# Kernel tuning notes

Measured on AMD Instinct MI355X. Metric: run time of the kernel, lower is better.

The kernel has to match this reference:

```python
import jax, jax.numpy as jnp
import numpy as np

CORNER_MASK = jnp.array(
    [[0, 0, 0], [0, 0, 1], [0, 1, 0], [0, 1, 1],
     [1, 0, 0], [1, 0, 1], [1, 1, 0], [1, 1, 1]], dtype=jnp.float32)


def setup_inputs() -> dict:
    key = jax.random.key(0)
    k1, k2, k3, k4 = jax.random.split(key, 4)
    DEPTH = 6
    G = 2 ** DEPTH            # 64 voxels per axis at depth 6
    C = 32                    # feature channels
    H = G * G * G             # 262144 octree nodes at depth 6
    N = 1_000_000             # query points (depth-7 node centers)

    data = jax.random.normal(k1, (1, C, H, 1), dtype=jnp.float32)
    # points scaled into [0, 2^depth]; last column is the batch id (single octree -> 0)
    xyz = jax.random.uniform(k2, (N, 3), dtype=jnp.float32) * G
    ids = jnp.zeros((N, 1), dtype=jnp.float32)
    pts = jnp.concatenate([xyz, ids], axis=1)

    # dense voxel -> node-index lookup emulating ocnn.octree_search_key;
    idx_grid = jax.random.randint(k3, (G, G, G), 0, H, dtype=jnp.int32)
    empty = jax.random.uniform(k4, (G, G, G)) < 0.1
    lut = jnp.where(empty, jnp.int32(-1), idx_grid)

    return {"data": data, "pts": pts, "lut": lut, "depth": DEPTH}


def reference(data, pts, lut, depth):
    # data: (1, C, H, 1); pts: (N, 4); lut: (G, G, G) int32; depth: python int
    G = 2 ** depth
    xyzf = pts[:, :3] - 0.5                      # (N, 3)
    xyzi = jnp.floor(xyzf)
    frac = xyzf - xyzi                           # (N, 3) fractional offsets

    corners = xyzi[:, None, :] + CORNER_MASK[None, :, :]   # (N, 8, 3)
    ci = corners.astype(jnp.int32)
    in_bounds = jnp.all((ci >= 0) & (ci < G), axis=-1)     # (N, 8)
    ci_safe = jnp.clip(ci, 0, G - 1)
    idx = lut[ci_safe[..., 0], ci_safe[..., 1], ci_safe[..., 2]]  # (N, 8)
    valid = in_bounds & (idx > -1)

    # trilinear weights: |prod((1 - mask) - frac)|, matching the torch code
    w = jnp.abs(jnp.prod((1.0 - CORNER_MASK)[None, :, :] - frac[:, None, :], axis=-1))
    w = jnp.where(valid, w, 0.0)                 # (N, 8)
    idx_safe = jnp.where(valid, idx, 0)

    feat = data[0, :, :, 0].T                    # (H, C)
    gathered = feat[idx_safe]                    # (N, 8, C)
    out = jnp.einsum('nk,nkc->nc', w, gathered)  # weighted accumulate
    norm = jnp.sum(w, axis=1, keepdims=True)     # (N, 1)
    out = out / (norm + 1e-10)
    return out.T[None, :, :, None]               # (1, C, N, 1)
```

## Files before the change

### kernel.cpp

```cpp
#include <hip/hip_runtime.h>
#include <hip/hip_fp16.h>


#define NCH 32

typedef float nvec4 __attribute__((ext_vector_type(4)));

__global__ __launch_bounds__(256) void octri_transpose_h(
    const float* __restrict__ data, __half* __restrict__ featH, int H) {
  __shared__ float tile[32][33];
  const int h0 = blockIdx.x * 32;
  const int tx = threadIdx.x;
  const int ty = threadIdx.y;
#pragma unroll
  for (int i = 0; i < 4; ++i) {
    int c = ty + 8 * i;
    tile[c][tx] =
        __builtin_nontemporal_load(&data[(size_t)c * H + h0 + tx]);
  }
  __syncthreads();
#pragma unroll
  for (int i = 0; i < 4; ++i) {
    int hl = ty + 8 * i;
    featH[(size_t)(h0 + hl) * NCH + tx] = __float2half(tile[tx][hl]);
  }
}

__global__ __launch_bounds__(256) void octri_voxelize(
    const __half* __restrict__ featH, const int* __restrict__ lut,
    __half* __restrict__ featV, unsigned long long* __restrict__ vmask) {
  const int t = threadIdx.x;
  const int zi = t >> 2;
  const int j = t & 3;
  const int v = blockIdx.x * 64 + zi;
  const int id = lut[v];

  nvec4 row = {0.f, 0.f, 0.f, 0.f};
  if (id >= 0)
    row = *(const nvec4*)(featH + ((size_t)id << 5) + (j << 3));
  *(nvec4*)(featV + ((size_t)v << 5) + (j << 3)) = row;

  const unsigned long long b = __ballot(id >= 0);
  unsigned int comp = 0;
#pragma unroll
  for (int k = 0; k < 16; ++k)
    comp |= ((unsigned)(b >> (4 * k)) & 1u) << k;
  __shared__ unsigned short sm16[4];
  if ((t & 63) == 0) sm16[t >> 6] = (unsigned short)comp;
  __syncthreads();
  if (t == 0) {
    unsigned long long m = (unsigned long long)sm16[0] |
                           ((unsigned long long)sm16[1] << 16) |
                           ((unsigned long long)sm16[2] << 32) |
                           ((unsigned long long)sm16[3] << 48);
    vmask[blockIdx.x] = m;
  }
}

__global__ __launch_bounds__(256) void octri_gather3(
    const __half* __restrict__ featV,
    const unsigned long long* __restrict__ vmask,
    const float* __restrict__ pts, const int* __restrict__ depth_p,
    float* __restrict__ out, int N) {
  __shared__ int meta[256][17];

  const int pblk = blockIdx.x * 256;
  const int G = 1 << depth_p[0];
  const int G1 = G - 1;

  {
    const int p = threadIdx.x;
    const int n = min(pblk + p, N - 1);
    const nvec4 pt =
        __builtin_nontemporal_load((const nvec4*)(pts + (size_t)n * 4));
    const float fx = pt.x - 0.5f, fy = pt.y - 0.5f, fz = pt.z - 0.5f;
    const float flx = floorf(fx), fly = floorf(fy), flz = floorf(fz);
    const int ix = (int)flx, iy = (int)fly, iz = (int)flz;
    const float rx = fx - flx, ry = fy - fly, rz = fz - flz;
    const float wx[2] = {1.f - rx, rx};
    const float wy[2] = {1.f - ry, ry};
    const float wz[2] = {1.f - rz, rz};
    const bool vx[2] = {(unsigned)ix < (unsigned)G,
                        (unsigned)(ix + 1) < (unsigned)G};
    const bool vy[2] = {(unsigned)iy < (unsigned)G,
                        (unsigned)(iy + 1) < (unsigned)G};
    const bool vz[2] = {(unsigned)iz < (unsigned)G,
                        (unsigned)(iz + 1) < (unsigned)G};
    const int cxc[2] = {min(max(ix, 0), G1), min(max(ix + 1, 0), G1)};
    const int cyc[2] = {min(max(iy, 0), G1), min(max(iy + 1, 0), G1)};
    const int czc[2] = {min(max(iz, 0), G1), min(max(iz + 1, 0), G1)};

    unsigned long long mrow[2][2];
#pragma unroll
    for (int bx = 0; bx < 2; ++bx)
#pragma unroll
      for (int by = 0; by < 2; ++by)
        mrow[bx][by] = vmask[cxc[bx] * G + cyc[by]];

    int vv[8];
    float w[8], wsum = 0.f;
#pragma unroll
    for (int k = 0; k < 8; ++k) {
      const int bx = (k >> 2) & 1, by = (k >> 1) & 1, bz = k & 1;
      const bool valid = vx[bx] && vy[by] && vz[bz] &&
                         (((mrow[bx][by] >> czc[bz]) & 1ull) != 0);
      vv[k] = (cxc[bx] * G + cyc[by]) * G + czc[bz];
      float wk = wx[bx] * wy[by] * wz[bz];
      wk = valid ? wk : 0.f;
      w[k] = wk;
      wsum += wk;
    }
    const float s = (pblk + p < N) ? (1.f / (wsum + 1e-10f)) : 0.f;
#pragma unroll
    for (int k = 0; k < 8; ++k) {
      meta[p][k] = vv[k];
      meta[p][8 + k] = __float_as_int(w[k] * s);
    }
  }
  __syncthreads();

  const int lane = threadIdx.x & 63;
  const int wid = threadIdx.x >> 6;
  const int j = lane & 3;
#pragma unroll
  for (int g = 0; g < 4; ++g) {
    const int p = (wid << 6) + (g << 4) + (lane >> 2);
    const int n = pblk + p;

    nvec4 r[8];
    float ws[8];
#pragma unroll
    for (int k = 0; k < 8; ++k) {
      const int v = meta[p][k];
      ws[k] = __int_as_float(meta[p][8 + k]);
      r[k] = *(const nvec4*)(featV + ((size_t)v << 5) + (j << 3));
    }
    float acc[8] = {};
#pragma unroll
    for (int k = 0; k < 8; ++k) {
      const __half2* h2 = (const __half2*)&r[k];
#pragma unroll
      for (int q = 0; q < 4; ++q) {
        const float2 f = __half22float2(h2[q]);
        acc[2 * q + 0] += ws[k] * f.x;
        acc[2 * q + 1] += ws[k] * f.y;
      }
    }
    if (n < N) {
#pragma unroll
      for (int q = 0; q < 8; ++q) {
        __builtin_nontemporal_store(acc[q],
                                    &out[(size_t)(8 * j + q) * N + n]);
      }
    }
  }
}

__global__ __launch_bounds__(256) void octri_gather2(
    const __half* __restrict__ featH,
    const float* __restrict__ pts, const int* __restrict__ lut,
    const int* __restrict__ depth_p, float* __restrict__ out, int N) {
  __shared__ int meta[256][17];
  const int pblk = blockIdx.x * 256;
  const int G = 1 << depth_p[0];

  {
    const int p = threadIdx.x;
    const int n = min(pblk + p, N - 1);
    const nvec4 pt =
        __builtin_nontemporal_load((const nvec4*)(pts + (size_t)n * 4));
    const float fx = pt.x - 0.5f, fy = pt.y - 0.5f, fz = pt.z - 0.5f;
    const float flx = floorf(fx), fly = floorf(fy), flz = floorf(fz);
    const int ix = (int)flx, iy = (int)fly, iz = (int)flz;
    const float rx = fx - flx, ry = fy - fly, rz = fz - flz;
    const float wx[2] = {1.f - rx, rx};
    const float wy[2] = {1.f - ry, ry};
    const float wz[2] = {1.f - rz, rz};
    const bool vx[2] = {(unsigned)ix < (unsigned)G,
                        (unsigned)(ix + 1) < (unsigned)G};
    const bool vy[2] = {(unsigned)iy < (unsigned)G,
                        (unsigned)(iy + 1) < (unsigned)G};
    const bool vz[2] = {(unsigned)iz < (unsigned)G,
                        (unsigned)(iz + 1) < (unsigned)G};

    int idx[8];
    float w[8], wsum = 0.f;
#pragma unroll
    for (int k = 0; k < 8; ++k) {
      const int bx = (k >> 2) & 1, by = (k >> 1) & 1, bz = k & 1;
      const bool inb = vx[bx] & vy[by] & vz[bz];
      int id = -1;
      if (inb)
        id = lut[((size_t)(ix + bx) * G + (iy + by)) * G + (iz + bz)];
      const bool valid = inb && (id > -1);
      float wk = wx[bx] * wy[by] * wz[bz];
      wk = valid ? wk : 0.f;
      idx[k] = valid ? id : 0;
      w[k] = wk;
      wsum += wk;
    }
    const float s = (pblk + p < N) ? (1.f / (wsum + 1e-10f)) : 0.f;
#pragma unroll
    for (int k = 0; k < 8; ++k) {
      meta[p][k] = idx[k];
      meta[p][8 + k] = __float_as_int(w[k] * s);
    }
  }
  __syncthreads();

  const int lane = threadIdx.x & 63;
  const int wid = threadIdx.x >> 6;
  const int j = lane & 3;
#pragma unroll
  for (int g = 0; g < 4; ++g) {
    const int p = (wid << 6) + (g << 4) + (lane >> 2);
    const int n = pblk + p;

    float acc[8] = {};
#pragma unroll
    for (int k = 0; k < 8; ++k) {
      const int id = meta[p][k];
      const float ws = __int_as_float(meta[p][8 + k]);
      const nvec4 hv = *(const nvec4*)(featH + (size_t)id * NCH + j * 8);
      const __half2* h2 = (const __half2*)&hv;
#pragma unroll
      for (int q = 0; q < 4; ++q) {
        const float2 f = __half22float2(h2[q]);
        acc[2 * q + 0] += ws * f.x;
        acc[2 * q + 1] += ws * f.y;
      }
    }
    if (n < N) {
#pragma unroll
      for (int q = 0; q < 8; ++q) {
        __builtin_nontemporal_store(acc[q],
                                    &out[(size_t)(8 * j + q) * N + n]);
      }
    }
  }
}

__global__ __launch_bounds__(256) void octri_gather_direct(
    const float* __restrict__ data, const float* __restrict__ pts,
    const int* __restrict__ lut, const int* __restrict__ depth_p,
    float* __restrict__ out, int N, int H) {
  const int n = blockIdx.x * blockDim.x + threadIdx.x;
  if (n >= N) return;
  const int G = 1 << depth_p[0];

  const float4 p = ((const float4*)pts)[n];
  const float fx = p.x - 0.5f, fy = p.y - 0.5f, fz = p.z - 0.5f;
  const float flx = floorf(fx), fly = floorf(fy), flz = floorf(fz);
  const int ix = (int)flx, iy = (int)fly, iz = (int)flz;
  const float rx = fx - flx, ry = fy - fly, rz = fz - flz;
  const float wx[2] = {1.f - rx, rx};
  const float wy[2] = {1.f - ry, ry};
  const float wz[2] = {1.f - rz, rz};

  int idx[8];
  float w[8], wsum = 0.f;
#pragma unroll
  for (int k = 0; k < 8; ++k) {
    const int bx = (k >> 2) & 1, by = (k >> 1) & 1, bz = k & 1;
    const int cx = ix + bx, cy = iy + by, cz = iz + bz;
    const bool inb = (cx >= 0) & (cx < G) & (cy >= 0) & (cy < G) &
                     (cz >= 0) & (cz < G);
    int id = -1;
    if (inb) id = lut[((size_t)cx * G + cy) * G + cz];
    const bool valid = inb && (id > -1);
    float wk = wx[bx] * wy[by] * wz[bz];
    wk = valid ? wk : 0.f;
    idx[k] = valid ? id : 0;
    w[k] = wk;
    wsum += wk;
  }

  const float s = 1.f / (wsum + 1e-10f);
#pragma unroll 4
  for (int c = 0; c < NCH; ++c) {
    const float* plane = data + (size_t)c * H;
    float a = 0.f;
#pragma unroll
    for (int k = 0; k < 8; ++k) a += w[k] * plane[idx[k]];
    out[(size_t)c * N + n] = a * s;
  }
}

extern "C" void kernel_launch(void* const* d_in, const int* in_sizes, int n_in,
                              void* d_out, int out_size, void* d_ws,
                              size_t ws_size, hipStream_t stream) {
  const float* data = (const float*)d_in[0];
  const float* pts = (const float*)d_in[1];
  const int* lut = (const int*)d_in[2];
  const int* depth_p = (const int*)d_in[3];
  float* out = (float*)d_out;

  const int H = in_sizes[0] / NCH;
  const int N = in_sizes[1] / 4;
  const int SV = in_sizes[2];

  int G = 1;
  while ((size_t)(G + 1) * (G + 1) * (G + 1) <= (size_t)SV) ++G;

  const size_t featH_bytes = (size_t)H * NCH * sizeof(__half);
  const size_t featV_bytes = (size_t)SV * NCH * sizeof(__half);
  const size_t needV = featV_bytes + (size_t)G * G * sizeof(unsigned long long);

  if (G == 64 && (size_t)G * G * G == (size_t)SV && (H % 32) == 0 &&
      ws_size >= needV &&
      featH_bytes <= (size_t)out_size * sizeof(float)) {
    __half* featH = (__half*)d_out;
    __half* featV = (__half*)d_ws;
    unsigned long long* vmask =
        (unsigned long long*)((char*)d_ws + featV_bytes);
    dim3 tb(32, 8);
    octri_transpose_h<<<H / 32, tb, 0, stream>>>(data, featH, H);
    octri_voxelize<<<SV / 64, 256, 0, stream>>>(featH, lut, featV, vmask);
    const int blocks = (N + 255) / 256;
    octri_gather3<<<blocks, 256, 0, stream>>>(featV, vmask, pts, depth_p,
                                              out, N);
  } else if (ws_size >= featH_bytes && (H % 32) == 0) {
    __half* featH = (__half*)d_ws;
    dim3 tb(32, 8);
    octri_transpose_h<<<H / 32, tb, 0, stream>>>(data, featH, H);
    const int blocks = (N + 255) / 256;
    octri_gather2<<<blocks, 256, 0, stream>>>(featH, pts, lut, depth_p, out,
                                              N);
  } else {
    octri_gather_direct<<<(N + 255) / 256, 256, 0, stream>>>(
        data, pts, lut, depth_p, out, N, H);
  }
}
```

Before: 261.6 us.

## Bin query points by x-slab before gathering to improve voxel cache locality

Adds a counting-sort pipeline (count, scan, scatter) that groups points into 8 x-slabs. The gather kernel then processes each slab so the featV rows it touches stay in a smaller working set, writing fp16 results to a temporary buffer. An unpermute kernel scatters the results back to the original order through LDS and writes the fp32 channel-major output. This trades several extra launches and extra passes over the points and temporary results for better cache hit rates on the random voxel gathers. The fp16 intermediate also adds rounding error.

```diff
diff --git a/kernel.cpp b/kernel.cpp
--- a/kernel.cpp
+++ b/kernel.cpp
@@ -3,6 +3,8 @@
 
 
 #define NCH 32
+#define BIN_W 512
+#define NGRP 8
 
 typedef float nvec4 __attribute__((ext_vector_type(4)));
 
@@ -15,8 +17,7 @@
 #pragma unroll
   for (int i = 0; i < 4; ++i) {
     int c = ty + 8 * i;
-    tile[c][tx] =
-        __builtin_nontemporal_load(&data[(size_t)c * H + h0 + tx]);
+    tile[c][tx] = __builtin_nontemporal_load(&data[(size_t)c * H + h0 + tx]);
   }
   __syncthreads();
 #pragma unroll
@@ -36,8 +37,7 @@
   const int id = lut[v];
 
   nvec4 row = {0.f, 0.f, 0.f, 0.f};
-  if (id >= 0)
-    row = *(const nvec4*)(featH + ((size_t)id << 5) + (j << 3));
+  if (id >= 0) row = *(const nvec4*)(featH + ((size_t)id << 5) + (j << 3));
   *(nvec4*)(featV + ((size_t)v << 5) + (j << 3)) = row;
 
   const unsigned long long b = __ballot(id >= 0);
@@ -57,17 +57,273 @@
   }
 }
 
+__global__ __launch_bounds__(256) void octri_bin_count(
+    const float* __restrict__ pts, int N, int NB, int* __restrict__ counts) {
+  __shared__ int cnt[NGRP];
+  if (threadIdx.x < NGRP) cnt[threadIdx.x] = 0;
+  __syncthreads();
+  const int b = blockIdx.x;
+#pragma unroll
+  for (int i = 0; i < 2; ++i) {
+    const int n = b * BIN_W + i * 256 + threadIdx.x;
+    if (n < N) {
+      const nvec4 pt =
+          __builtin_nontemporal_load((const nvec4*)(pts + (size_t)n * 4));
+      const int ix = (int)floorf(pt.x - 0.5f);
+      const int g = min(max(ix, 0), 63) >> 3;
+      atomicAdd(&cnt[g], 1);
+    }
+  }
+  __syncthreads();
+  if (threadIdx.x < NGRP) counts[threadIdx.x * NB + b] = cnt[threadIdx.x];
+}
+
+__global__ __launch_bounds__(256) void octri_bin_scan(
+    const int* __restrict__ counts, int* __restrict__ bases, int M) {
+  extern __shared__ int buf[];
+  const int t = threadIdx.x;
+  const int seg = (M + 255) / 256;
+  for (int i = t; i < M; i += 256) buf[i] = counts[i];
+  __syncthreads();
+  int* stot = buf + M;
+  {
+    int s = 0;
+    const int lo = t * seg, hi = min(lo + seg, M);
+    for (int i = lo; i < hi; ++i) { int c = buf[i]; buf[i] = s; s += c; }
+    stot[t] = s;
+  }
+  __syncthreads();
+  if (t == 0) {
+    int s = 0;
+    for (int i = 0; i < 256; ++i) { int c = stot[i]; stot[i] = s; s += c; }
+  }
+  __syncthreads();
+  {
+    const int add = stot[t];
+    const int lo = t * seg, hi = min(lo + seg, M);
+    for (int i = lo; i < hi; ++i) bases[i] = buf[i] + add;
+  }
+}
+
+__global__ __launch_bounds__(256) void octri_bin_scatter(
+    const float* __restrict__ pts, int N, int NB, const int* __restrict__ bases,
+    float* __restrict__ binned, int* __restrict__ inv) {
+  __shared__ int run[NGRP];
+  __shared__ int wcnt[4][NGRP];
+  __shared__ int woff[4][NGRP];
+  const int b = blockIdx.x;
+  const int t = threadIdx.x;
+  const int lane = t & 63, wid = t >> 6;
+  if (t < NGRP) run[t] = bases[t * NB + b];
+  __syncthreads();
+#pragma unroll
+  for (int i = 0; i < 2; ++i) {
+    if (t < 32) wcnt[t >> 3][t & 7] = 0;
+    __syncthreads();
+    const int n = b * BIN_W + i * 256 + t;
+    const bool act = (n < N);
+    nvec4 pt = {0.f, 0.f, 0.f, 0.f};
+    int g = 0;
+    if (act) {
+      pt = __builtin_nontemporal_load((const nvec4*)(pts + (size_t)n * 4));
+      g = min(max((int)floorf(pt.x - 0.5f), 0), 63) >> 3;
+    }
+    unsigned long long m = 0;
+#pragma unroll
+    for (int gg = 0; gg < NGRP; ++gg) {
+      const unsigned long long bm = __ballot(act && (g == gg));
+      if (gg == g) m = bm;
+    }
+    const unsigned long long ltm = (1ull << lane) - 1ull;
+    const int rank = __popcll(m & ltm);
+    if (act && rank == 0) wcnt[wid][g] = __popcll(m);
+    __syncthreads();
+    if (t < NGRP) {
+      int r = run[t];
+#pragma unroll
+      for (int w = 0; w < 4; ++w) { woff[w][t] = r; r += wcnt[w][t]; }
+      run[t] = r;
+    }
+    __syncthreads();
+    if (act) {
+      const int slot = woff[wid][g] + rank;
+      __builtin_nontemporal_store(pt, (nvec4*)(binned + (size_t)slot * 4));
+      inv[n] = slot;
+    }
+    __syncthreads();
+  }
+}
+
+__global__ __launch_bounds__(256) void octri_gather4(
+    const __half* __restrict__ featV, const unsigned long long* __restrict__ vmask,
+    const float* __restrict__ binned, const int* __restrict__ bases, int NB,
+    int N, int CPB, __half* __restrict__ temp) {
+  __shared__ int meta[256][17];
+  const int g = blockIdx.x & 7;
+  const int Gb0 = bases[g * NB];
+  const int Gb1 = (g < 7) ? bases[(g + 1) * NB] : N;
+  const int G = 64, G1 = 63;
+
+  for (int chunk = blockIdx.x >> 3;; chunk += CPB) {
+    const int s0 = Gb0 + (chunk << 8);
+    if (s0 >= Gb1) break;
+    const int cnt = min(256, Gb1 - s0);
+
+    {
+      const int p = threadIdx.x;
+      const int s = s0 + min(p, cnt - 1);
+      const nvec4 pt =
+          __builtin_nontemporal_load((const nvec4*)(binned + (size_t)s * 4));
+      const float fx = pt.x - 0.5f, fy = pt.y - 0.5f, fz = pt.z - 0.5f;
+      const float flx = floorf(fx), fly = floorf(fy), flz = floorf(fz);
+      const int ix = (int)flx, iy = (int)fly, iz = (int)flz;
+      const float rx = fx - flx, ry = fy - fly, rz = fz - flz;
+      const float wx[2] = {1.f - rx, rx};
+      const float wy[2] = {1.f - ry, ry};
+      const float wz[2] = {1.f - rz, rz};
+      const bool vx[2] = {(unsigned)ix < (unsigned)G,
+                          (unsigned)(ix + 1) < (unsigned)G};
+      const bool vy[2] = {(unsigned)iy < (unsigned)G,
+                          (unsigned)(iy + 1) < (unsigned)G};
+      const bool vz[2] = {(unsigned)iz < (unsigned)G,
+                          (unsigned)(iz + 1) < (unsigned)G};
+      const int cxc[2] = {min(max(ix, 0), G1), min(max(ix + 1, 0), G1)};
+      const int cyc[2] = {min(max(iy, 0), G1), min(max(iy + 1, 0), G1)};
+      const int czc[2] = {min(max(iz, 0), G1), min(max(iz + 1, 0), G1)};
+
+      unsigned long long mrow[2][2];
+#pragma unroll
+      for (int bx = 0; bx < 2; ++bx)
+#pragma unroll
+        for (int by = 0; by < 2; ++by)
+          mrow[bx][by] = vmask[cxc[bx] * G + cyc[by]];
+
+      int vv[8];
+      float w[8], wsum = 0.f;
+#pragma unroll
+      for (int k = 0; k < 8; ++k) {
+        const int bx = (k >> 2) & 1, by = (k >> 1) & 1, bz = k & 1;
+        const bool valid = vx[bx] && vy[by] && vz[bz] &&
+                           (((mrow[bx][by] >> czc[bz]) & 1ull) != 0);
+        vv[k] = (cxc[bx] * G + cyc[by]) * G + czc[bz];
+        float wk = wx[bx] * wy[by] * wz[bz];
+        wk = valid ? wk : 0.f;
+        w[k] = wk;
+        wsum += wk;
+      }
+      const float sc = (p < cnt) ? (1.f / (wsum + 1e-10f)) : 0.f;
+#pragma unroll
+      for (int k = 0; k < 8; ++k) {
+        meta[p][k] = vv[k];
+        meta[p][8 + k] = __float_as_int(w[k] * sc);
+      }
+    }
+    __syncthreads();
+
+    const int lane = threadIdx.x & 63;
+    const int wid = threadIdx.x >> 6;
+    const int j = lane & 3;
+#pragma unroll
+    for (int gq = 0; gq < 4; ++gq) {
+      const int p = (wid << 6) + (gq << 4) + (lane >> 2);
+
+      nvec4 r[8];
+      float ws[8];
+#pragma unroll
+      for (int k = 0; k < 8; ++k) {
+        const int v = meta[p][k];
+        ws[k] = __int_as_float(meta[p][8 + k]);
+        r[k] = *(const nvec4*)(featV + ((size_t)v << 5) + (j << 3));
+      }
+      float acc[8] = {};
+#pragma unroll
+      for (int k = 0; k < 8; ++k) {
+        const __half2* h2 = (const __half2*)&r[k];
+#pragma unroll
+        for (int q = 0; q < 4; ++q) {
+          const float2 f = __half22float2(h2[q]);
+          acc[2 * q + 0] += ws[k] * f.x;
+          acc[2 * q + 1] += ws[k] * f.y;
+        }
+      }
+      if (p < cnt) {
+        union { __half2 h2[4]; nvec4 v; } u;
+#pragma unroll
+        for (int q = 0; q < 4; ++q)
+          u.h2[q] = __floats2half2_rn(acc[2 * q], acc[2 * q + 1]);
+        __builtin_nontemporal_store(
+            u.v, (nvec4*)(temp + ((size_t)(s0 + p) << 5) + (j << 3)));
+      }
+    }
+    __syncthreads();
+  }
+}
+
+__global__ __launch_bounds__(256) void octri_unpermute(
+    const __half* __restrict__ temp, const int* __restrict__ inv,
+    const int* __restrict__ bases, int NB, int N, float* __restrict__ out) {
+  __shared__ __half rows[BIN_W * NCH];
+  __shared__ int cur[NGRP], off[NGRP + 1], Gb[NGRP + 1];
+  const int b = blockIdx.x;
+  const int t = threadIdx.x;
+  if (t < NGRP) {
+    const int c0 = bases[t * NB + b];
+    const int c1 = (b + 1 < NB) ? bases[t * NB + b + 1]
+                                : ((t < 7) ? bases[(t + 1) * NB] : N);
+    cur[t] = c0;
+    off[t] = c1 - c0;
+    Gb[t] = bases[t * NB];
+  }
+  if (t == 0) Gb[NGRP] = N;
+  __syncthreads();
+  if (t == 0) {
+    int s = 0;
+#pragma unroll
+    for (int gg = 0; gg < NGRP; ++gg) { int l = off[gg]; off[gg] = s; s += l; }
+    off[NGRP] = s;
+  }
+  __syncthreads();
+  for (int gg = 0; gg < NGRP; ++gg) {
+    const int len4 = (off[gg + 1] - off[gg]) << 2;
+    const nvec4* src = (const nvec4*)(temp + ((size_t)cur[gg] << 5));
+    nvec4* dst = (nvec4*)(rows + ((size_t)off[gg] << 5));
+    for (int k = t; k < len4; k += 256)
+      dst[k] = __builtin_nontemporal_load(src + k);
+  }
+  __syncthreads();
+#pragma unroll
+  for (int i = 0; i < 2; ++i) {
+    const int n = b * BIN_W + i * 256 + t;
+    if (n < N) {
+      const int slot = inv[n];
+      int gg = 0;
+      while (slot >= Gb[gg + 1]) ++gg;
+      const int r = slot - cur[gg] + off[gg];
+      const __half* hp = rows + ((size_t)r << 5);
+#pragma unroll
+      for (int k = 0; k < 4; ++k) {
+        const nvec4 hv = *(const nvec4*)(hp + (k << 3));
+        const __half2* h2 = (const __half2*)&hv;
+#pragma unroll
+        for (int q = 0; q < 4; ++q) {
+          const float2 f = __half22float2(h2[q]);
+          __builtin_nontemporal_store(f.x, &out[(size_t)(k * 8 + 2 * q) * N + n]);
+          __builtin_nontemporal_store(f.y,
+                                      &out[(size_t)(k * 8 + 2 * q + 1) * N + n]);
+        }
+      }
+    }
+  }
+}
+
 __global__ __launch_bounds__(256) void octri_gather3(
-    const __half* __restrict__ featV,
-    const unsigned long long* __restrict__ vmask,
+    const __half* __restrict__ featV, const unsigned long long* __restrict__ vmask,
     const float* __restrict__ pts, const int* __restrict__ depth_p,
     float* __restrict__ out, int N) {
   __shared__ int meta[256][17];
-
   const int pblk = blockIdx.x * 256;
   const int G = 1 << depth_p[0];
   const int G1 = G - 1;
-
   {
     const int p = threadIdx.x;
     const int n = min(pblk + p, N - 1);
@@ -89,14 +345,12 @@
     const int cxc[2] = {min(max(ix, 0), G1), min(max(ix + 1, 0), G1)};
     const int cyc[2] = {min(max(iy, 0), G1), min(max(iy + 1, 0), G1)};
     const int czc[2] = {min(max(iz, 0), G1), min(max(iz + 1, 0), G1)};
-
     unsigned long long mrow[2][2];
 #pragma unroll
     for (int bx = 0; bx < 2; ++bx)
 #pragma unroll
       for (int by = 0; by < 2; ++by)
         mrow[bx][by] = vmask[cxc[bx] * G + cyc[by]];
-
     int vv[8];
     float w[8], wsum = 0.f;
 #pragma unroll
@@ -118,7 +372,6 @@
     }
   }
   __syncthreads();
-
   const int lane = threadIdx.x & 63;
   const int wid = threadIdx.x >> 6;
   const int j = lane & 3;
@@ -126,7 +379,6 @@
   for (int g = 0; g < 4; ++g) {
     const int p = (wid << 6) + (g << 4) + (lane >> 2);
     const int n = pblk + p;
-
     nvec4 r[8];
     float ws[8];
 #pragma unroll
@@ -148,94 +400,8 @@
     }
     if (n < N) {
 #pragma unroll
-      for (int q = 0; q < 8; ++q) {
-        __builtin_nontemporal_store(acc[q],
-                                    &out[(size_t)(8 * j + q) * N + n]);
-      }
-    }
-  }
-}
-
-__global__ __launch_bounds__(256) void octri_gather2(
-    const __half* __restrict__ featH,
-    const float* __restrict__ pts, const int* __restrict__ lut,
-    const int* __restrict__ depth_p, float* __restrict__ out, int N) {
-  __shared__ int meta[256][17];
-  const int pblk = blockIdx.x * 256;
-  const int G = 1 << depth_p[0];
-
-  {
-    const int p = threadIdx.x;
-    const int n = min(pblk + p, N - 1);
-    const nvec4 pt =
-        __builtin_nontemporal_load((const nvec4*)(pts + (size_t)n * 4));
-    const float fx = pt.x - 0.5f, fy = pt.y - 0.5f, fz = pt.z - 0.5f;
-    const float flx = floorf(fx), fly = floorf(fy), flz = floorf(fz);
-    const int ix = (int)flx, iy = (int)fly, iz = (int)flz;
-    const float rx = fx - flx, ry = fy - fly, rz = fz - flz;
-    const float wx[2] = {1.f - rx, rx};
-    const float wy[2] = {1.f - ry, ry};
-    const float wz[2] = {1.f - rz, rz};
-    const bool vx[2] = {(unsigned)ix < (unsigned)G,
-                        (unsigned)(ix + 1) < (unsigned)G};
-    const bool vy[2] = {(unsigned)iy < (unsigned)G,
-                        (unsigned)(iy + 1) < (unsigned)G};
-    const bool vz[2] = {(unsigned)iz < (unsigned)G,
-                        (unsigned)(iz + 1) < (unsigned)G};
-
-    int idx[8];
-    float w[8], wsum = 0.f;
-#pragma unroll
-    for (int k = 0; k < 8; ++k) {
-      const int bx = (k >> 2) & 1, by = (k >> 1) & 1, bz = k & 1;
-      const bool inb = vx[bx] & vy[by] & vz[bz];
-      int id = -1;
-      if (inb)
-        id = lut[((size_t)(ix + bx) * G + (iy + by)) * G + (iz + bz)];
-      const bool valid = inb && (id > -1);
-      float wk = wx[bx] * wy[by] * wz[bz];
-      wk = valid ? wk : 0.f;
-      idx[k] = valid ? id : 0;
-      w[k] = wk;
-      wsum += wk;
-    }
-    const float s = (pblk + p < N) ? (1.f / (wsum + 1e-10f)) : 0.f;
-#pragma unroll
-    for (int k = 0; k < 8; ++k) {
-      meta[p][k] = idx[k];
-      meta[p][8 + k] = __float_as_int(w[k] * s);
-    }
-  }
-  __syncthreads();
-
-  const int lane = threadIdx.x & 63;
-  const int wid = threadIdx.x >> 6;
-  const int j = lane & 3;
-#pragma unroll
-  for (int g = 0; g < 4; ++g) {
-    const int p = (wid << 6) + (g << 4) + (lane >> 2);
-    const int n = pblk + p;
-
-    float acc[8] = {};
-#pragma unroll
-    for (int k = 0; k < 8; ++k) {
-      const int id = meta[p][k];
-      const float ws = __int_as_float(meta[p][8 + k]);
-      const nvec4 hv = *(const nvec4*)(featH + (size_t)id * NCH + j * 8);
-      const __half2* h2 = (const __half2*)&hv;
-#pragma unroll
-      for (int q = 0; q < 4; ++q) {
-        const float2 f = __half22float2(h2[q]);
-        acc[2 * q + 0] += ws * f.x;
-        acc[2 * q + 1] += ws * f.y;
-      }
-    }
-    if (n < N) {
-#pragma unroll
-      for (int q = 0; q < 8; ++q) {
-        __builtin_nontemporal_store(acc[q],
-                                    &out[(size_t)(8 * j + q) * N + n]);
-      }
+      for (int q = 0; q < 8; ++q)
+        __builtin_nontemporal_store(acc[q], &out[(size_t)(8 * j + q) * N + n]);
     }
   }
 }
@@ -247,7 +413,6 @@
   const int n = blockIdx.x * blockDim.x + threadIdx.x;
   if (n >= N) return;
   const int G = 1 << depth_p[0];
-
   const float4 p = ((const float4*)pts)[n];
   const float fx = p.x - 0.5f, fy = p.y - 0.5f, fz = p.z - 0.5f;
   const float flx = floorf(fx), fly = floorf(fy), flz = floorf(fz);
@@ -256,15 +421,14 @@
   const float wx[2] = {1.f - rx, rx};
   const float wy[2] = {1.f - ry, ry};
   const float wz[2] = {1.f - rz, rz};
-
   int idx[8];
   float w[8], wsum = 0.f;
 #pragma unroll
   for (int k = 0; k < 8; ++k) {
     const int bx = (k >> 2) & 1, by = (k >> 1) & 1, bz = k & 1;
     const int cx = ix + bx, cy = iy + by, cz = iz + bz;
-    const bool inb = (cx >= 0) & (cx < G) & (cy >= 0) & (cy < G) &
-                     (cz >= 0) & (cz < G);
+    const bool inb = (cx >= 0) & (cx < G) & (cy >= 0) & (cy < G) & (cz >= 0) &
+                     (cz < G);
     int id = -1;
     if (inb) id = lut[((size_t)cx * G + cy) * G + cz];
     const bool valid = inb && (id > -1);
@@ -274,7 +438,6 @@
     w[k] = wk;
     wsum += wk;
   }
-
   const float s = 1.f / (wsum + 1e-10f);
 #pragma unroll 4
   for (int c = 0; c < NCH; ++c) {
@@ -302,13 +465,58 @@
   int G = 1;
   while ((size_t)(G + 1) * (G + 1) * (G + 1) <= (size_t)SV) ++G;
 
+  const int NB = (N + BIN_W - 1) / BIN_W;
+  const int M = NGRP * NB;
+
   const size_t featH_bytes = (size_t)H * NCH * sizeof(__half);
   const size_t featV_bytes = (size_t)SV * NCH * sizeof(__half);
-  const size_t needV = featV_bytes + (size_t)G * G * sizeof(unsigned long long);
+
+  size_t offw = 0;
+  auto alloc = [&](size_t bytes) {
+    offw = (offw + 255) & ~(size_t)255;
+    size_t o = offw;
+    offw += bytes;
+    return o;
+  };
+  const size_t o_featV = alloc(featV_bytes);
+  const size_t o_vmask = alloc((size_t)G * G * sizeof(unsigned long long));
+  const size_t o_binned = alloc((size_t)NB * BIN_W * 16);
+  const size_t o_temp = alloc((size_t)NB * BIN_W * NCH * sizeof(__half));
+  const size_t o_inv = alloc((size_t)NB * BIN_W * sizeof(int));
+  const size_t o_counts = alloc((size_t)M * sizeof(int));
+  const size_t o_bases = alloc((size_t)M * sizeof(int));
+  const size_t need_full = offw;
+
+  const size_t scan_lds = (size_t)(M + 256) * sizeof(int);
+  const size_t needV =
+      featV_bytes + (size_t)G * G * sizeof(unsigned long long);
 
   if (G == 64 && (size_t)G * G * G == (size_t)SV && (H % 32) == 0 &&
-      ws_size >= needV &&
+      ws_size >= need_full && scan_lds <= 150 * 1024 &&
       featH_bytes <= (size_t)out_size * sizeof(float)) {
+    char* ws = (char*)d_ws;
+    __half* featH = (__half*)d_out;
+    __half* featV = (__half*)(ws + o_featV);
+    unsigned long long* vmask = (unsigned long long*)(ws + o_vmask);
+    float* binned = (float*)(ws + o_binned);
+    __half* temp = (__half*)(ws + o_temp);
+    int* inv = (int*)(ws + o_inv);
+    int* counts = (int*)(ws + o_counts);
+    int* bases = (int*)(ws + o_bases);
+
+    dim3 tb(32, 8);
+    octri_transpose_h<<<H / 32, tb, 0, stream>>>(data, featH, H);
+    octri_voxelize<<<SV / 64, 256, 0, stream>>>(featH, lut, featV, vmask);
+    octri_bin_count<<<NB, 256, 0, stream>>>(pts, N, NB, counts);
+    octri_bin_scan<<<1, 256, scan_lds, stream>>>(counts, bases, M);
+    octri_bin_scatter<<<NB, 256, 0, stream>>>(pts, N, NB, bases, binned, inv);
+    const int CPB = (N / NGRP + 1024) / 1024 * 5 + 8;
+    octri_gather4<<<NGRP * CPB, 256, 0, stream>>>(featV, vmask, binned, bases,
+                                                  NB, N, CPB, temp);
+    octri_unpermute<<<NB, 256, 0, stream>>>(temp, inv, bases, NB, N, out);
+  } else if (G == 64 && (size_t)G * G * G == (size_t)SV && (H % 32) == 0 &&
+             ws_size >= needV &&
+             featH_bytes <= (size_t)out_size * sizeof(float)) {
     __half* featH = (__half*)d_out;
     __half* featV = (__half*)d_ws;
     unsigned long long* vmask =
@@ -316,16 +524,8 @@
     dim3 tb(32, 8);
     octri_transpose_h<<<H / 32, tb, 0, stream>>>(data, featH, H);
     octri_voxelize<<<SV / 64, 256, 0, stream>>>(featH, lut, featV, vmask);
-    const int blocks = (N + 255) / 256;
-    octri_gather3<<<blocks, 256, 0, stream>>>(featV, vmask, pts, depth_p,
-                                              out, N);
-  } else if (ws_size >= featH_bytes && (H % 32) == 0) {
-    __half* featH = (__half*)d_ws;
-    dim3 tb(32, 8);
-    octri_transpose_h<<<H / 32, tb, 0, stream>>>(data, featH, H);
-    const int blocks = (N + 255) / 256;
-    octri_gather2<<<blocks, 256, 0, stream>>>(featH, pts, lut, depth_p, out,
-                                              N);
+    octri_gather3<<<(N + 255) / 256, 256, 0, stream>>>(featV, vmask, pts,
+                                                       depth_p, out, N);
   } else {
     octri_gather_direct<<<(N + 255) / 256, 256, 0, stream>>>(
         data, pts, lut, depth_p, out, N, H);
```

Measured after the change: 267.2 us. +2.1%, slower.
